# Kernel optimization log

Hardware: AMD Instinct MI355X
Metric: run time of the kernel (lower is better)

## Reference

```python
import jax, jax.numpy as jnp
import numpy as np

C = 256

def setup_inputs() -> dict:
    key = jax.random.key(0)
    ks = jax.random.split(key, 9)
    B, H, W = 32, 32, 32
    s = C ** -0.5  # init scale for weights
    inputs = jax.random.normal(ks[0], (B, H, W, C), jnp.float32)
    Wq = jax.random.normal(ks[1], (C, C), jnp.float32) * s
    Wk = jax.random.normal(ks[2], (C, C), jnp.float32) * s
    Wv = jax.random.normal(ks[3], (C, C), jnp.float32) * s
    Wo = jax.random.normal(ks[4], (C, C), jnp.float32) * s
    bq = jnp.zeros((C,), jnp.float32)
    bk = jnp.zeros((C,), jnp.float32)
    bv = jnp.zeros((C,), jnp.float32)
    bo = jnp.zeros((C,), jnp.float32)
    return {"inputs": inputs, "Wq": Wq, "bq": bq, "Wk": Wk, "bk": bk,
            "Wv": Wv, "bv": bv, "Wo": Wo, "bo": bo}

def reference(inputs, Wq, bq, Wk, bk, Wv, bv, Wo, bo):
    B, H, W, c = inputs.shape
    scale = jnp.float32(c) ** -0.5
    x = inputs.reshape(B, H * W, c)           # 1x1 conv == per-pixel matmul
    q = x @ Wq + bq                           # [B, HW, C]
    k = x @ Wk + bk
    v = x @ Wv + bv
    scores = jnp.einsum('bnc,bmc->bnm', q, k) * scale  # [B, HW, HW]
    attn = jax.nn.softmax(scores, axis=-1)
    attended = jnp.einsum('bnm,bmc->bnc', attn, v)     # [B, HW, C]
    out = attended @ Wo + bo
    return out.reshape(B, H, W, c)
```

## Files before the change

kernel.cpp:

```cpp
#include <hip/hip_runtime.h>
#include <hip/hip_bf16.h>

typedef __bf16 bf16;
typedef __bf16 bf16x4 __attribute__((ext_vector_type(4)));
typedef __bf16 bf16x8 __attribute__((ext_vector_type(8)));
typedef float f32x4 __attribute__((ext_vector_type(4)));

#define SM_C 0.09016994374947424f

__global__ __launch_bounds__(256) void transpose_w(
    const float* __restrict__ Wq, const float* __restrict__ Wk,
    const float* __restrict__ Wv, const float* __restrict__ Wo,
    bf16* __restrict__ Wt)
{
    int idx = blockIdx.x * 256 + threadIdx.x;
    int m = idx >> 16, r = idx & 65535;
    int n = r >> 8, k = r & 255;
    const float* W = (m == 0) ? Wq : (m == 1) ? Wk : (m == 2) ? Wv : Wo;
    Wt[(size_t)m * 65536 + n * 256 + k] = (bf16)W[k * 256 + n];
}

__global__ __launch_bounds__(256, 3) void qkv_gemm(
    const float* __restrict__ X, const bf16* __restrict__ Wt,
    const float* __restrict__ bq, const float* __restrict__ bk,
    const float* __restrict__ bv,
    bf16* __restrict__ Qo, bf16* __restrict__ Ko, bf16* __restrict__ Vto)
{
    __shared__ bf16 Xs[128 * 72];
    __shared__ bf16 Ws_[128 * 72];

    const int t    = threadIdx.x;
    const int lane = t & 63, wv = t >> 6;
    const int quad = lane >> 4, l16 = lane & 15;
    const int bm   = blockIdx.x;
    const int bn   = blockIdx.y;
    const int proj = bn >> 1;

    const bf16* W = Wt + (size_t)proj * 65536 + (size_t)(bn & 1) * 32768;
    const float* bias = (proj == 0) ? bq : (proj == 1) ? bk : bv;

    const int m0 = t >> 3;
    const int c0 = (t & 7) * 8;

    const f32x4 zero = {0.0f, 0.0f, 0.0f, 0.0f};
    f32x4 acc[2][8];
#pragma unroll
    for (int i = 0; i < 2; ++i)
#pragma unroll
        for (int j = 0; j < 8; ++j) acc[i][j] = zero;

    f32x4 xa[4], xb[4]; bf16x8 wp[4];
#pragma unroll
    for (int p = 0; p < 4; ++p) {
        const float* px = X + (size_t)(bm * 128 + m0 + p * 32) * 256 + c0;
        xa[p] = *(const f32x4*)px; xb[p] = *(const f32x4*)(px + 4);
        wp[p] = *(const bf16x8*)(W + (size_t)(m0 + p * 32) * 256 + c0);
    }

    for (int kt = 0; kt < 4; ++kt) {
#pragma unroll
        for (int p = 0; p < 4; ++p) {
            bf16x8 r;
#pragma unroll
            for (int j = 0; j < 4; ++j) { r[j] = (bf16)xa[p][j]; r[j + 4] = (bf16)xb[p][j]; }
            *(bf16x8*)(Xs + (m0 + p * 32) * 72 + c0) = r;
            *(bf16x8*)(Ws_ + (m0 + p * 32) * 72 + c0) = wp[p];
        }
        __syncthreads();

        if (kt < 3) {
#pragma unroll
            for (int p = 0; p < 4; ++p) {
                const float* px = X + (size_t)(bm * 128 + m0 + p * 32) * 256 + (kt + 1) * 64 + c0;
                xa[p] = *(const f32x4*)px; xb[p] = *(const f32x4*)(px + 4);
                wp[p] = *(const bf16x8*)(W + (size_t)(m0 + p * 32) * 256 + (kt + 1) * 64 + c0);
            }
        }

#pragma unroll
        for (int ks = 0; ks < 2; ++ks) {
            bf16x8 a[2], bb[8];
#pragma unroll
            for (int mt = 0; mt < 2; ++mt)
                a[mt] = *(const bf16x8*)(Xs + (wv * 32 + mt * 16 + l16) * 72 + ks * 32 + quad * 8);
#pragma unroll
            for (int nt = 0; nt < 8; ++nt)
                bb[nt] = *(const bf16x8*)(Ws_ + (nt * 16 + l16) * 72 + ks * 32 + quad * 8);
#pragma unroll
            for (int mt = 0; mt < 2; ++mt)
#pragma unroll
                for (int nt = 0; nt < 8; ++nt)
                    acc[mt][nt] = __builtin_amdgcn_mfma_f32_16x16x32_bf16(
                        a[mt], bb[nt], acc[mt][nt], 0, 0, 0);
        }
        __syncthreads();
    }

#pragma unroll
    for (int nt = 0; nt < 8; ++nt) {
        int col = (bn & 1) * 128 + nt * 16 + l16;
        float bvv = bias[col];
#pragma unroll
        for (int mt = 0; mt < 2; ++mt) {
            int grow0 = bm * 128 + wv * 32 + mt * 16 + quad * 4;
            if (proj == 2) {
                bf16x4 pk;
#pragma unroll
                for (int r = 0; r < 4; ++r) pk[r] = (bf16)(acc[mt][nt][r] + bvv);
                int b = grow0 >> 10, m = grow0 & 1023;
                *(bf16x4*)(Vto + (size_t)b * 262144 + (size_t)col * 1024 + m) = pk;
            } else {
                bf16* dst = (proj == 0) ? Qo : Ko;
#pragma unroll
                for (int r = 0; r < 4; ++r)
                    dst[(size_t)(grow0 + r) * 256 + col] = (bf16)(acc[mt][nt][r] + bvv);
            }
        }
    }
}

__global__ __launch_bounds__(512, 2) void flash_attn(
    const bf16* __restrict__ Qr, const bf16* __restrict__ K,
    const bf16* __restrict__ Vt, bf16* __restrict__ A)
{
    __shared__ bf16 Ks[2][32 * 264];
    __shared__ bf16 Vs[2][256 * 40];
    __shared__ bf16 Ps[8][16 * 32];

    const int t    = threadIdx.x;
    const int lane = t & 63, wv = t >> 6;
    const int quad = lane >> 4, l16 = lane & 15;
    const int b  = blockIdx.x;
    const int qt = blockIdx.y;

    bf16x8 qf[8];
    const size_t qrow = (size_t)b * 1024 + qt * 128 + wv * 16 + l16;
#pragma unroll
    for (int ks = 0; ks < 8; ++ks)
        qf[ks] = *(const bf16x8*)(Qr + qrow * 256 + ks * 32 + quad * 8);

    const f32x4 zero = {0.0f, 0.0f, 0.0f, 0.0f};
    f32x4 o[16];
#pragma unroll
    for (int n = 0; n < 16; ++n) o[n] = zero;
    float lst[4] = {0.f, 0.f, 0.f, 0.f};

    char* Pb = (char*)(Ps[wv]);

    const int kv0 = t >> 4, kc0 = (t & 15) * 8;
    const int vc0 = t >> 1, vm0 = (t & 1) * 8;

    bf16x8 kp[2], vp[2];
#pragma unroll
    for (int p = 0; p < 2; ++p) {
        kp[p] = *(const bf16x8*)(K + (size_t)(b * 1024 + kv0) * 256 + kc0 + p * 128);
        vp[p] = *(const bf16x8*)(Vt + (size_t)b * 262144 + (size_t)vc0 * 1024 + vm0 + p * 16);
    }
#pragma unroll
    for (int p = 0; p < 2; ++p) {
        *(bf16x8*)(Ks[0] + kv0 * 264 + kc0 + p * 128) = kp[p];
        *(bf16x8*)(Vs[0] + vc0 * 40 + vm0 + p * 16) = vp[p];
    }
#pragma unroll
    for (int p = 0; p < 2; ++p) {
        kp[p] = *(const bf16x8*)(K + (size_t)(b * 1024 + 32 + kv0) * 256 + kc0 + p * 128);
        vp[p] = *(const bf16x8*)(Vt + (size_t)b * 262144 + (size_t)vc0 * 1024 + 32 + vm0 + p * 16);
    }

    for (int j = 0; j < 32; ++j) {
        const bf16* Kb = Ks[j & 1];
        const bf16* Vb = Vs[j & 1];
        __syncthreads();

        f32x4 s[2];
        s[0] = zero; s[1] = zero;
        __builtin_amdgcn_s_setprio(1);
#pragma unroll
        for (int ks = 0; ks < 8; ++ks) {
#pragma unroll
            for (int n = 0; n < 2; ++n) {
                bf16x8 bfr = *(const bf16x8*)(Kb + (n * 16 + l16) * 264 + ks * 32 + quad * 8);
                s[n] = __builtin_amdgcn_mfma_f32_16x16x32_bf16(qf[ks], bfr, s[n], 0, 0, 0);
            }
        }
        __builtin_amdgcn_s_setprio(0);

        if (j < 31) {
            bf16* Kn = Ks[(j + 1) & 1];
            bf16* Vn = Vs[(j + 1) & 1];
#pragma unroll
            for (int p = 0; p < 2; ++p) {
                *(bf16x8*)(Kn + kv0 * 264 + kc0 + p * 128) = kp[p];
                *(bf16x8*)(Vn + vc0 * 40 + vm0 + p * 16) = vp[p];
            }
            if (j < 30) {
#pragma unroll
                for (int p = 0; p < 2; ++p) {
                    kp[p] = *(const bf16x8*)(K + (size_t)(b * 1024 + (j + 2) * 32 + kv0) * 256 + kc0 + p * 128);
                    vp[p] = *(const bf16x8*)(Vt + (size_t)b * 262144 + (size_t)vc0 * 1024 + (j + 2) * 32 + vm0 + p * 16);
                }
            }
        }

#pragma unroll
        for (int n = 0; n < 2; ++n) {
#pragma unroll
            for (int r = 0; r < 4; ++r) {
                float pv = __builtin_amdgcn_exp2f(s[n][r] * SM_C);
                lst[r] += pv;
                int row = quad * 4 + r;
                *(bf16*)(Pb + ((row * 64 + n * 32 + l16 * 2) ^ ((row & 7) << 4))) = (bf16)pv;
            }
        }

        bf16x8 af = *(const bf16x8*)(Pb + ((l16 * 64 + quad * 16) ^ ((l16 & 7) << 4)));
        __builtin_amdgcn_s_setprio(1);
#pragma unroll
        for (int n = 0; n < 16; ++n) {
            bf16x8 bfr = *(const bf16x8*)(Vb + (n * 16 + l16) * 40 + quad * 8);
            o[n] = __builtin_amdgcn_mfma_f32_16x16x32_bf16(af, bfr, o[n], 0, 0, 0);
        }
        __builtin_amdgcn_s_setprio(0);
    }

#pragma unroll
    for (int r = 0; r < 4; ++r) {
        float l = lst[r];
        for (int off = 1; off < 16; off <<= 1)
            l += __shfl_xor(l, off, 64);
        float inv = 1.0f / l;
        size_t grow = (size_t)b * 1024 + qt * 128 + wv * 16 + quad * 4 + r;
#pragma unroll
        for (int n = 0; n < 16; ++n)
            A[grow * 256 + n * 16 + l16] = (bf16)(o[n][r] * inv);
    }
}

__global__ __launch_bounds__(256) void oproj_gemm(
    const bf16* __restrict__ Xv, const bf16* __restrict__ W,
    const float* __restrict__ bias, float* __restrict__ outv)
{
    __shared__ bf16 Xs[128 * 72];
    __shared__ bf16 Ws[64 * 72];

    const int t    = threadIdx.x;
    const int lane = t & 63, wv = t >> 6;
    const int quad = lane >> 4, l16 = lane & 15;
    const int bm = blockIdx.x;
    const int bn = blockIdx.y;

    const f32x4 zero = {0.0f, 0.0f, 0.0f, 0.0f};
    f32x4 acc[2][4];
    for (int i = 0; i < 2; ++i)
        for (int j = 0; j < 4; ++j) acc[i][j] = zero;

    const int m0 = t >> 3;
    const int c0 = (t & 7) * 8;

    bf16x8 xp[4], wp[2];
#pragma unroll
    for (int p = 0; p < 4; ++p)
        xp[p] = *(const bf16x8*)(Xv + (size_t)(bm * 128 + m0 + p * 32) * 256 + c0);
#pragma unroll
    for (int p = 0; p < 2; ++p)
        wp[p] = *(const bf16x8*)(W + (size_t)(bn * 64 + m0 + p * 32) * 256 + c0);

    for (int kt = 0; kt < 4; ++kt) {
#pragma unroll
        for (int p = 0; p < 4; ++p)
            *(bf16x8*)(Xs + (m0 + p * 32) * 72 + c0) = xp[p];
#pragma unroll
        for (int p = 0; p < 2; ++p)
            *(bf16x8*)(Ws + (m0 + p * 32) * 72 + c0) = wp[p];
        __syncthreads();

        if (kt < 3) {
#pragma unroll
            for (int p = 0; p < 4; ++p)
                xp[p] = *(const bf16x8*)(Xv + (size_t)(bm * 128 + m0 + p * 32) * 256 + (kt + 1) * 64 + c0);
#pragma unroll
            for (int p = 0; p < 2; ++p)
                wp[p] = *(const bf16x8*)(W + (size_t)(bn * 64 + m0 + p * 32) * 256 + (kt + 1) * 64 + c0);
        }

#pragma unroll
        for (int ks = 0; ks < 2; ++ks) {
            bf16x8 a[2], bb[4];
            for (int mt = 0; mt < 2; ++mt)
                a[mt] = *(const bf16x8*)(Xs + (wv * 32 + mt * 16 + l16) * 72 + ks * 32 + quad * 8);
            for (int nt = 0; nt < 4; ++nt)
                bb[nt] = *(const bf16x8*)(Ws + (nt * 16 + l16) * 72 + ks * 32 + quad * 8);
            for (int mt = 0; mt < 2; ++mt)
                for (int nt = 0; nt < 4; ++nt)
                    acc[mt][nt] = __builtin_amdgcn_mfma_f32_16x16x32_bf16(
                        a[mt], bb[nt], acc[mt][nt], 0, 0, 0);
        }
        __syncthreads();
    }

#pragma unroll
    for (int nt = 0; nt < 4; ++nt) {
        int col = bn * 64 + nt * 16 + l16;
        float bvv = bias[col];
#pragma unroll
        for (int mt = 0; mt < 2; ++mt)
#pragma unroll
            for (int r = 0; r < 4; ++r) {
                int grow = bm * 128 + wv * 32 + mt * 16 + quad * 4 + r;
                outv[(size_t)grow * 256 + col] = acc[mt][nt][r] + bvv;
            }
    }
}

extern "C" void kernel_launch(void* const* d_in, const int* in_sizes, int n_in,
                              void* d_out, int out_size, void* d_ws, size_t ws_size,
                              hipStream_t stream)
{
    (void)in_sizes; (void)n_in; (void)out_size; (void)ws_size;
    const float* X  = (const float*)d_in[0];
    const float* Wq = (const float*)d_in[1];
    const float* bq = (const float*)d_in[2];
    const float* Wk = (const float*)d_in[3];
    const float* bk = (const float*)d_in[4];
    const float* Wv = (const float*)d_in[5];
    const float* bv = (const float*)d_in[6];
    const float* Wo = (const float*)d_in[7];
    const float* bo = (const float*)d_in[8];
    float* out = (float*)d_out;

    const size_t NTOK = (size_t)32768 * 256;

    bf16* Wt  = (bf16*)d_ws;
    bf16* Qw  = (bf16*)d_ws + 262144;
    bf16* Kw  = Qw + NTOK;
    bf16* Vtw = Kw + NTOK;

    transpose_w<<<1024, 256, 0, stream>>>(Wq, Wk, Wv, Wo, Wt);
    qkv_gemm   <<<dim3(256, 6), 256, 0, stream>>>(X, Wt, bq, bk, bv, Qw, Kw, Vtw);
    flash_attn <<<dim3(32, 8),  512, 0, stream>>>(Qw, Kw, Vtw, Qw);
    oproj_gemm <<<dim3(256, 4), 256, 0, stream>>>(Qw, Wt + 3 * 65536, bo, out);
}
```

Before: 187.7 us.

## Fuse output projection into flash-attention epilogue via shared memory

The separate oproj_gemm kernel is removed. Each attention block now normalizes its 128x256 output tile into LDS, loads Wo in two 128-column halves into LDS, and computes the projection plus bias directly to the fp32 output. This avoids writing the attention result to global memory, reading it back, and paying one kernel launch. The cost is a single large static LDS buffer (about 139 KB) reused for the K/V/P staging and the epilogue, which limits each CU to one block, plus a per-block reload of Wo. The s_setprio hints around the MFMA loops are also dropped.

Measured after the change: 181.8 us. -3.1%, faster.

```diff
diff --git a/kernel.cpp b/kernel.cpp
--- a/kernel.cpp
+++ b/kernel.cpp
@@ -121,11 +121,16 @@
 
 __global__ __launch_bounds__(512, 2) void flash_attn(
     const bf16* __restrict__ Qr, const bf16* __restrict__ K,
-    const bf16* __restrict__ Vt, bf16* __restrict__ A)
+    const bf16* __restrict__ Vt, const bf16* __restrict__ Wo,
+    const float* __restrict__ bo, float* __restrict__ out)
 {
-    __shared__ bf16 Ks[2][32 * 264];
-    __shared__ bf16 Vs[2][256 * 40];
-    __shared__ bf16 Ps[8][16 * 32];
+    __shared__ __align__(16) char smem[142336];
+    bf16* const Ksp0 = (bf16*)(smem);
+    bf16* const Ksp1 = (bf16*)(smem + 16896);
+    bf16* const Vsp0 = (bf16*)(smem + 33792);
+    bf16* const Vsp1 = (bf16*)(smem + 54272);
+    bf16* const Os   = (bf16*)(smem);
+    bf16* const Wos  = (bf16*)(smem + 74752);
 
     const int t    = threadIdx.x;
     const int lane = t & 63, wv = t >> 6;
@@ -133,6 +138,8 @@
     const int b  = blockIdx.x;
     const int qt = blockIdx.y;
 
+    char* const Pb = smem + 74752 + wv * 1024;
+
     bf16x8 qf[8];
     const size_t qrow = (size_t)b * 1024 + qt * 128 + wv * 16 + l16;
 #pragma unroll
@@ -144,8 +151,6 @@
 #pragma unroll
     for (int n = 0; n < 16; ++n) o[n] = zero;
     float lst[4] = {0.f, 0.f, 0.f, 0.f};
-
-    char* Pb = (char*)(Ps[wv]);
 
     const int kv0 = t >> 4, kc0 = (t & 15) * 8;
     const int vc0 = t >> 1, vm0 = (t & 1) * 8;
@@ -158,8 +163,8 @@
     }
 #pragma unroll
     for (int p = 0; p < 2; ++p) {
-        *(bf16x8*)(Ks[0] + kv0 * 264 + kc0 + p * 128) = kp[p];
-        *(bf16x8*)(Vs[0] + vc0 * 40 + vm0 + p * 16) = vp[p];
+        *(bf16x8*)(Ksp0 + kv0 * 264 + kc0 + p * 128) = kp[p];
+        *(bf16x8*)(Vsp0 + vc0 * 40 + vm0 + p * 16) = vp[p];
     }
 #pragma unroll
     for (int p = 0; p < 2; ++p) {
@@ -168,13 +173,12 @@
     }
 
     for (int j = 0; j < 32; ++j) {
-        const bf16* Kb = Ks[j & 1];
-        const bf16* Vb = Vs[j & 1];
+        const bf16* Kb = (j & 1) ? Ksp1 : Ksp0;
+        const bf16* Vb = (j & 1) ? Vsp1 : Vsp0;
         __syncthreads();
 
         f32x4 s[2];
         s[0] = zero; s[1] = zero;
-        __builtin_amdgcn_s_setprio(1);
 #pragma unroll
         for (int ks = 0; ks < 8; ++ks) {
 #pragma unroll
@@ -183,11 +187,10 @@
                 s[n] = __builtin_amdgcn_mfma_f32_16x16x32_bf16(qf[ks], bfr, s[n], 0, 0, 0);
             }
         }
-        __builtin_amdgcn_s_setprio(0);
 
         if (j < 31) {
-            bf16* Kn = Ks[(j + 1) & 1];
-            bf16* Vn = Vs[(j + 1) & 1];
+            bf16* Kn = (j & 1) ? Ksp0 : Ksp1;
+            bf16* Vn = (j & 1) ? Vsp0 : Vsp1;
 #pragma unroll
             for (int p = 0; p < 2; ++p) {
                 *(bf16x8*)(Kn + kv0 * 264 + kc0 + p * 128) = kp[p];
@@ -214,101 +217,80 @@
         }
 
         bf16x8 af = *(const bf16x8*)(Pb + ((l16 * 64 + quad * 16) ^ ((l16 & 7) << 4)));
-        __builtin_amdgcn_s_setprio(1);
 #pragma unroll
         for (int n = 0; n < 16; ++n) {
             bf16x8 bfr = *(const bf16x8*)(Vb + (n * 16 + l16) * 40 + quad * 8);
             o[n] = __builtin_amdgcn_mfma_f32_16x16x32_bf16(af, bfr, o[n], 0, 0, 0);
         }
-        __builtin_amdgcn_s_setprio(0);
-    }
-
+    }
+
+    __syncthreads();
+
+    float inv[4];
 #pragma unroll
     for (int r = 0; r < 4; ++r) {
         float l = lst[r];
+#pragma unroll
         for (int off = 1; off < 16; off <<= 1)
             l += __shfl_xor(l, off, 64);
-        float inv = 1.0f / l;
-        size_t grow = (size_t)b * 1024 + qt * 128 + wv * 16 + quad * 4 + r;
-#pragma unroll
-        for (int n = 0; n < 16; ++n)
-            A[grow * 256 + n * 16 + l16] = (bf16)(o[n][r] * inv);
-    }
-}
-
-__global__ __launch_bounds__(256) void oproj_gemm(
-    const bf16* __restrict__ Xv, const bf16* __restrict__ W,
-    const float* __restrict__ bias, float* __restrict__ outv)
-{
-    __shared__ bf16 Xs[128 * 72];
-    __shared__ bf16 Ws[64 * 72];
-
-    const int t    = threadIdx.x;
-    const int lane = t & 63, wv = t >> 6;
-    const int quad = lane >> 4, l16 = lane & 15;
-    const int bm = blockIdx.x;
-    const int bn = blockIdx.y;
-
-    const f32x4 zero = {0.0f, 0.0f, 0.0f, 0.0f};
-    f32x4 acc[2][4];
-    for (int i = 0; i < 2; ++i)
-        for (int j = 0; j < 4; ++j) acc[i][j] = zero;
-
-    const int m0 = t >> 3;
-    const int c0 = (t & 7) * 8;
-
-    bf16x8 xp[4], wp[2];
-#pragma unroll
-    for (int p = 0; p < 4; ++p)
-        xp[p] = *(const bf16x8*)(Xv + (size_t)(bm * 128 + m0 + p * 32) * 256 + c0);
-#pragma unroll
-    for (int p = 0; p < 2; ++p)
-        wp[p] = *(const bf16x8*)(W + (size_t)(bn * 64 + m0 + p * 32) * 256 + c0);
-
-    for (int kt = 0; kt < 4; ++kt) {
-#pragma unroll
-        for (int p = 0; p < 4; ++p)
-            *(bf16x8*)(Xs + (m0 + p * 32) * 72 + c0) = xp[p];
-#pragma unroll
-        for (int p = 0; p < 2; ++p)
-            *(bf16x8*)(Ws + (m0 + p * 32) * 72 + c0) = wp[p];
+        inv[r] = 1.0f / l;
+    }
+#pragma unroll
+    for (int n = 0; n < 16; ++n)
+#pragma unroll
+        for (int r = 0; r < 4; ++r)
+            Os[(wv * 16 + quad * 4 + r) * 264 + n * 16 + l16] = (bf16)(o[n][r] * inv[r]);
+
+    const int rh = (wv & 1) * 64;
+    const int nq = wv >> 1;
+    const size_t orow0 = (size_t)b * 1024 + qt * 128 + rh;
+
+#pragma unroll
+    for (int h = 0; h < 2; ++h) {
+        if (h) __syncthreads();
+#pragma unroll
+        for (int i = 0; i < 8; ++i) {
+            int c = t + i * 512;
+            int row = c >> 5, c8 = (c & 31) * 8;
+            *(bf16x8*)(Wos + row * 264 + c8) =
+                *(const bf16x8*)(Wo + (size_t)(h * 128 + row) * 256 + c8);
+        }
         __syncthreads();
 
-        if (kt < 3) {
-#pragma unroll
-            for (int p = 0; p < 4; ++p)
-                xp[p] = *(const bf16x8*)(Xv + (size_t)(bm * 128 + m0 + p * 32) * 256 + (kt + 1) * 64 + c0);
-#pragma unroll
-            for (int p = 0; p < 2; ++p)
-                wp[p] = *(const bf16x8*)(W + (size_t)(bn * 64 + m0 + p * 32) * 256 + (kt + 1) * 64 + c0);
-        }
-
-#pragma unroll
-        for (int ks = 0; ks < 2; ++ks) {
-            bf16x8 a[2], bb[4];
-            for (int mt = 0; mt < 2; ++mt)
-                a[mt] = *(const bf16x8*)(Xs + (wv * 32 + mt * 16 + l16) * 72 + ks * 32 + quad * 8);
-            for (int nt = 0; nt < 4; ++nt)
-                bb[nt] = *(const bf16x8*)(Ws + (nt * 16 + l16) * 72 + ks * 32 + quad * 8);
-            for (int mt = 0; mt < 2; ++mt)
-                for (int nt = 0; nt < 4; ++nt)
+        f32x4 acc[4][2];
+#pragma unroll
+        for (int mt = 0; mt < 4; ++mt) { acc[mt][0] = zero; acc[mt][1] = zero; }
+
+#pragma unroll
+        for (int ks = 0; ks < 8; ++ks) {
+            bf16x8 a[4], bb[2];
+#pragma unroll
+            for (int mt = 0; mt < 4; ++mt)
+                a[mt] = *(const bf16x8*)(Os + (rh + mt * 16 + l16) * 264 + ks * 32 + quad * 8);
+#pragma unroll
+            for (int nt = 0; nt < 2; ++nt)
+                bb[nt] = *(const bf16x8*)(Wos + (nq * 32 + nt * 16 + l16) * 264 + ks * 32 + quad * 8);
+#pragma unroll
+            for (int mt = 0; mt < 4; ++mt)
+#pragma unroll
+                for (int nt = 0; nt < 2; ++nt)
                     acc[mt][nt] = __builtin_amdgcn_mfma_f32_16x16x32_bf16(
                         a[mt], bb[nt], acc[mt][nt], 0, 0, 0);
         }
-        __syncthreads();
-    }
-
-#pragma unroll
-    for (int nt = 0; nt < 4; ++nt) {
-        int col = bn * 64 + nt * 16 + l16;
-        float bvv = bias[col];
-#pragma unroll
-        for (int mt = 0; mt < 2; ++mt)
-#pragma unroll
-            for (int r = 0; r < 4; ++r) {
-                int grow = bm * 128 + wv * 32 + mt * 16 + quad * 4 + r;
-                outv[(size_t)grow * 256 + col] = acc[mt][nt][r] + bvv;
-            }
+
+#pragma unroll
+        for (int nt = 0; nt < 2; ++nt) {
+            int col = h * 128 + nq * 32 + nt * 16 + l16;
+            float bvv = bo[col];
+#pragma unroll
+            for (int mt = 0; mt < 4; ++mt) {
+#pragma unroll
+                for (int r = 0; r < 4; ++r) {
+                    size_t row = orow0 + mt * 16 + quad * 4 + r;
+                    out[row * 256 + col] = acc[mt][nt][r] + bvv;
+                }
+            }
+        }
     }
 }
 
@@ -337,6 +319,5 @@
 
     transpose_w<<<1024, 256, 0, stream>>>(Wq, Wk, Wv, Wo, Wt);
     qkv_gemm   <<<dim3(256, 6), 256, 0, stream>>>(X, Wt, bq, bk, bv, Qw, Kw, Vtw);
-    flash_attn <<<dim3(32, 8),  512, 0, stream>>>(Qw, Kw, Vtw, Qw);
-    oproj_gemm <<<dim3(256, 4), 256, 0, stream>>>(Qw, Wt + 3 * 65536, bo, out);
+    flash_attn <<<dim3(32, 8),  512, 0, stream>>>(Qw, Kw, Vtw, Wt + 3 * 65536, bo, out);
 }
```
